# Optimization experiments

Measured on AMD Instinct MI355X. Metric: run time of the kernel, lower is better.

Reference implementation:

```python
import jax, jax.numpy as jnp
import numpy as np
import math

K = 4          # wavelet polynomial order
C = 16         # channel multiplier
MODES = 64     # retained Fourier modes (alpha)
L_LEVEL = 0    # coarsest level
B_SZ, N_SZ = 32, 8192
CK = C * K


def _get_filter_legendre(k):
    """Pure-numpy port of get_filter(base='legendre', k): Alpert multiwavelet filters."""
    from numpy.polynomial import legendre as npleg
    Poly = np.polynomial.Polynomial
    phi_coeff = np.zeros((k, k))
    phi_2x_coeff = np.zeros((k, k))
    for ki in range(k):
        c = np.zeros(ki + 1); c[ki] = 1.0
        base = Poly(npleg.leg2poly(c))
        p1 = base(Poly([-1.0, 2.0])).coef
        p2 = base(Poly([-1.0, 4.0])).coef
        phi_coeff[ki, :len(p1)] = np.sqrt(2 * ki + 1) * p1
        phi_2x_coeff[ki, :len(p2)] = np.sqrt(2.0) * np.sqrt(2 * ki + 1) * p2

    def proj_half(a, b, upper):
        # integral of poly(a)*poly(b) over [0,0.5] (upper=False) or [0.5,1] (upper=True)
        prod = np.convolve(a, b)
        prod[np.abs(prod) < 1e-8] = 0.0
        n = np.arange(len(prod))
        w = ((1.0 - np.power(0.5, n + 1)) if upper else np.power(0.5, n + 1)) / (n + 1)
        return (prod * w).sum()

    psi1_coeff = np.zeros((k, k)); psi2_coeff = np.zeros((k, k))
    for ki in range(k):
        psi1_coeff[ki, :] = phi_2x_coeff[ki, :]
        for i in range(k):
            p = proj_half(phi_2x_coeff[ki, :ki + 1], phi_coeff[i, :i + 1], False)
            psi1_coeff[ki, :] -= p * phi_coeff[i, :]
            psi2_coeff[ki, :] -= p * phi_coeff[i, :]
        for j in range(ki):
            p = proj_half(phi_2x_coeff[ki, :ki + 1], psi1_coeff[j, :], False)
            psi1_coeff[ki, :] -= p * psi1_coeff[j, :]
            psi2_coeff[ki, :] -= p * psi2_coeff[j, :]
        norm1 = proj_half(psi1_coeff[ki, :], psi1_coeff[ki, :], False)
        norm2 = proj_half(psi2_coeff[ki, :], psi2_coeff[ki, :], True)
        nrm = np.sqrt(norm1 + norm2)
        psi1_coeff[ki, :] /= nrm; psi2_coeff[ki, :] /= nrm
        psi1_coeff[np.abs(psi1_coeff) < 1e-8] = 0.0
        psi2_coeff[np.abs(psi2_coeff) < 1e-8] = 0.0

    t, w = npleg.leggauss(k)
    x_m = (t + 1.0) / 2.0; wm = w / 2.0     # Gauss-Legendre on [0,1]
    pv = np.polynomial.polynomial.polyval
    phi = lambda i, x: pv(x, phi_coeff[i])
    def psi(i, x):
        m = (x <= 0.5).astype(np.float64)
        return pv(x, psi1_coeff[i]) * m + pv(x, psi2_coeff[i]) * (1 - m)
    H0 = np.zeros((k, k)); H1 = np.zeros((k, k)); G0 = np.zeros((k, k)); G1 = np.zeros((k, k))
    s2 = np.sqrt(2.0)
    for ki in range(k):
        for kpi in range(k):
            H0[ki, kpi] = (wm * phi(ki, x_m / 2) * phi(kpi, x_m)).sum() / s2
            G0[ki, kpi] = (wm * psi(ki, x_m / 2) * phi(kpi, x_m)).sum() / s2
            H1[ki, kpi] = (wm * phi(ki, (x_m + 1) / 2) * phi(kpi, x_m)).sum() / s2
            G1[ki, kpi] = (wm * psi(ki, (x_m + 1) / 2) * phi(kpi, x_m)).sum() / s2
    for M in (H0, H1, G0, G1):
        M[np.abs(M) < 1e-8] = 0.0
    return H0, H1, G0, G1


_H0, _H1, _G0, _G1 = _get_filter_legendre(K)
# PHI0 = PHI1 = I for legendre, so H0r = H0 etc.
EC_S = jnp.asarray(np.concatenate((_H0.T, _H1.T), axis=0), dtype=jnp.float32)  # [2k,k]
EC_D = jnp.asarray(np.concatenate((_G0.T, _G1.T), axis=0), dtype=jnp.float32)
RC_E = jnp.asarray(np.concatenate((_H0, _G0), axis=0), dtype=jnp.float32)
RC_O = jnp.asarray(np.concatenate((_H1, _G1), axis=0), dtype=jnp.float32)


def _skft(x, w_re, w_im):
    """sparseKernelFT1d: FFT, truncated per-mode complex matmul, inverse FFT."""
    B, N, c, k = x.shape
    w = w_re + 1j * w_im                                   # [ck, ck, modes]
    xf = jnp.fft.rfft(x.reshape(B, N, c * k), axis=1)       # [B, N//2+1, ck]
    l = min(w.shape[-1], N // 2 + 1)
    out = jnp.einsum('bxi,iox->bxo', xf[:, :l, :], w[:, :, :l])
    out_full = jnp.zeros((B, N // 2 + 1, c * k), dtype=out.dtype).at[:, :l, :].set(out)
    y = jnp.fft.irfft(out_full, n=N, axis=1)
    return y.reshape(B, N, c, k)


def _mwt_cz1d(x, wA_re, wA_im, wB_re, wB_im, wC_re, wC_im, t0_w, t0_b):
    B, N, c, k = x.shape
    ns = int(math.floor(math.log2(N)))
    Ud, Us = [], []
    for _ in range(ns - L_LEVEL):
        # wavelet_transform
        xa = jnp.concatenate([x[:, ::2], x[:, 1::2]], axis=-1)   # [B, N/2, c, 2k]
        d = xa @ EC_D
        x = xa @ EC_S
        Ud.append(_skft(d, wA_re, wA_im) + _skft(x, wB_re, wB_im))
        Us.append(_skft(d, wC_re, wC_im))
    x = x @ t0_w.T + t0_b                                        # T0 linear on last dim k
    for i in range(ns - 1 - L_LEVEL, -1, -1):
        x = x + Us[i]
        x = jnp.concatenate([x, Ud[i]], axis=-1)                 # [B, M, c, 2k]
        x_e = x @ RC_E
        x_o = x @ RC_O
        M = x_e.shape[1]
        # interleave even/odd along the length axis
        x = jnp.stack([x_e, x_o], axis=2).reshape(B, 2 * M, c, k)
    return x


def setup_inputs() -> dict:
    key = jax.random.key(0)
    ks = jax.random.split(key, 8)
    scale = 1.0 / (CK * CK)
    return {
        'x': jax.random.normal(ks[0], (B_SZ, N_SZ, C, K), dtype=jnp.float32),
        'wA_re': scale * jax.random.uniform(ks[1], (CK, CK, MODES), dtype=jnp.float32),
        'wA_im': scale * jax.random.uniform(ks[2], (CK, CK, MODES), dtype=jnp.float32),
        'wB_re': scale * jax.random.uniform(ks[3], (CK, CK, MODES), dtype=jnp.float32),
        'wB_im': scale * jax.random.uniform(ks[4], (CK, CK, MODES), dtype=jnp.float32),
        'wC_re': scale * jax.random.uniform(ks[5], (CK, CK, MODES), dtype=jnp.float32),
        'wC_im': scale * jax.random.uniform(ks[6], (CK, CK, MODES), dtype=jnp.float32),
        't0_w': jax.random.normal(ks[7], (K, K), dtype=jnp.float32) / np.sqrt(K).astype(np.float32),
        't0_b': jnp.zeros((K,), dtype=jnp.float32),
    }


def reference(x, wA_re, wA_im, wB_re, wB_im, wC_re, wC_im, t0_w, t0_b):
    return _mwt_cz1d(x, wA_re, wA_im, wB_re, wB_im, wC_re, wC_im, t0_w, t0_b)
```

## Files before the change

kernel.cpp:

```cpp
#include <hip/hip_runtime.h>
#include <cmath>
#include <cstdint>


typedef __attribute__((ext_vector_type(8))) short bf16x8;
typedef __attribute__((ext_vector_type(4))) float f32x4;

struct Mat84 { float v[8][4]; };
struct Ptrs6 { const float* src[6]; uint16_t* dst[6]; };
struct TwLvls {
  int blkOff[14]; int Nl[13]; int l[13];
  unsigned long long fOff[13]; unsigned long long iOff[13];
};
struct FwdLvls {
  int blkOff[14]; int K[13]; int Kchunk[13];
  unsigned long long fOff[13]; unsigned long long bOff[13]; unsigned long long dOff[13];
};
struct MidLvls {
  int blkOff[14]; int l[13]; int nz[13];
  unsigned long long dOff[13]; unsigned long long sOff[13];
};
struct InvLvls {
  int blkOff[14]; int Nl[13]; int K2l[13];
  unsigned long long iOff[13]; unsigned long long sOff[13]; unsigned long long uOff[13];
};
struct DeepD { unsigned long long dsbOff[13]; };
struct DeepR { unsigned long long uOff[13]; };

__device__ __host__ inline uint16_t f2bf(float f) {
  union { float f; uint32_t u; } cv; cv.f = f;
  uint32_t u = cv.u;
  return (uint16_t)((u + 0x7fffu + ((u >> 16) & 1u)) >> 16);
}
__device__ inline float bf2f(uint16_t h) { return __uint_as_float((uint32_t)h << 16); }
__device__ inline uint32_t pack2(float a, float b) {
  return (uint32_t)f2bf(a) | ((uint32_t)f2bf(b) << 16);
}
__device__ inline bf16x8 negbf(bf16x8 x) {
  bf16x8 r;
#pragma unroll
  for (int j = 0; j < 8; j++) r[j] = (short)(x[j] ^ (short)0x8000);
  return r;
}
__device__ inline void gld_lds16(const uint16_t* g, uint16_t* l) {
  __builtin_amdgcn_global_load_lds(
      (const __attribute__((address_space(1))) void*)g,
      (__attribute__((address_space(3))) void*)l, 16, 0, 0);
}

static double proj_half_h(const double* a, const double* b, bool upper) {
  double prod[7] = {0, 0, 0, 0, 0, 0, 0};
  for (int i = 0; i < 4; i++)
    for (int j = 0; j < 4; j++)
      prod[i + j] += a[i] * b[j];
  for (int n = 0; n < 7; n++)
    if (fabs(prod[n]) < 1e-8) prod[n] = 0.0;
  double s = 0.0;
  for (int n = 0; n < 7; n++) {
    double w = upper ? (1.0 - pow(0.5, n + 1)) / (n + 1) : pow(0.5, n + 1) / (n + 1);
    s += prod[n] * w;
  }
  return s;
}
static double polyval4(const double* c, double x) {
  return c[0] + x * (c[1] + x * (c[2] + x * c[3]));
}

static void compute_filters(Mat84& ecs, Mat84& ecd, Mat84& rce, Mat84& rco) {
  const double leg[4][4] = {{1, 0, 0, 0}, {0, 1, 0, 0}, {-0.5, 0, 1.5, 0}, {0, -1.5, 0, 2.5}};
  double phi_c[4][4] = {}, phi2x_c[4][4] = {};
  const double s2 = sqrt(2.0);
  for (int ki = 0; ki < 4; ki++) {
    double a[4] = {0, 0, 0, 0};
    for (int j = 3; j >= 0; j--) {
      double na[4];
      for (int t = 0; t < 4; t++) { double v = -a[t]; if (t > 0) v += 2.0 * a[t - 1]; na[t] = v; }
      na[0] += leg[ki][j];
      for (int t = 0; t < 4; t++) a[t] = na[t];
    }
    for (int t = 0; t < 4; t++) phi_c[ki][t] = sqrt(2.0 * ki + 1.0) * a[t];
    double bb[4] = {0, 0, 0, 0};
    for (int j = 3; j >= 0; j--) {
      double nb[4];
      for (int t = 0; t < 4; t++) { double v = -bb[t]; if (t > 0) v += 4.0 * bb[t - 1]; nb[t] = v; }
      nb[0] += leg[ki][j];
      for (int t = 0; t < 4; t++) bb[t] = nb[t];
    }
    for (int t = 0; t < 4; t++) phi2x_c[ki][t] = s2 * sqrt(2.0 * ki + 1.0) * bb[t];
  }
  double psi1[4][4] = {}, psi2[4][4] = {};
  for (int ki = 0; ki < 4; ki++) {
    for (int t = 0; t < 4; t++) { psi1[ki][t] = phi2x_c[ki][t]; psi2[ki][t] = 0.0; }
    for (int i = 0; i < 4; i++) {
      double p = proj_half_h(phi2x_c[ki], phi_c[i], false);
      for (int t = 0; t < 4; t++) { psi1[ki][t] -= p * phi_c[i][t]; psi2[ki][t] -= p * phi_c[i][t]; }
    }
    for (int j = 0; j < ki; j++) {
      double p = proj_half_h(phi2x_c[ki], psi1[j], false);
      for (int t = 0; t < 4; t++) { psi1[ki][t] -= p * psi1[j][t]; psi2[ki][t] -= p * psi2[j][t]; }
    }
    double n1 = proj_half_h(psi1[ki], psi1[ki], false);
    double n2 = proj_half_h(psi2[ki], psi2[ki], true);
    double nr = sqrt(n1 + n2);
    for (int t = 0; t < 4; t++) { psi1[ki][t] /= nr; psi2[ki][t] /= nr; }
    for (int t = 0; t < 4; t++) {
      if (fabs(psi1[ki][t]) < 1e-8) psi1[ki][t] = 0.0;
      if (fabs(psi2[ki][t]) < 1e-8) psi2[ki][t] = 0.0;
    }
  }
  const double tq[4] = {-0.8611363115940526, -0.3399810435848563,
                        0.3399810435848563, 0.8611363115940526};
  const double wq[4] = {0.34785484513745385, 0.6521451548625461,
                        0.6521451548625461, 0.34785484513745385};
  double H0[4][4], H1[4][4], G0[4][4], G1[4][4];
  for (int ki = 0; ki < 4; ki++)
    for (int kp = 0; kp < 4; kp++) {
      double h0 = 0, h1 = 0, g0 = 0, g1 = 0;
      for (int m = 0; m < 4; m++) {
        double xm = (tq[m] + 1.0) * 0.5, wm = wq[m] * 0.5;
        double pk = polyval4(phi_c[kp], xm);
        h0 += wm * polyval4(phi_c[ki], xm * 0.5) * pk;
        h1 += wm * polyval4(phi_c[ki], (xm + 1.0) * 0.5) * pk;
        g0 += wm * polyval4(psi1[ki], xm * 0.5) * pk;
        g1 += wm * polyval4(psi2[ki], (xm + 1.0) * 0.5) * pk;
      }
      H0[ki][kp] = h0 / s2; H1[ki][kp] = h1 / s2; G0[ki][kp] = g0 / s2; G1[ki][kp] = g1 / s2;
    }
  for (int i = 0; i < 4; i++)
    for (int j = 0; j < 4; j++) {
      if (fabs(H0[i][j]) < 1e-8) H0[i][j] = 0.0;
      if (fabs(H1[i][j]) < 1e-8) H1[i][j] = 0.0;
      if (fabs(G0[i][j]) < 1e-8) G0[i][j] = 0.0;
      if (fabs(G1[i][j]) < 1e-8) G1[i][j] = 0.0;
    }
  for (int j = 0; j < 4; j++)
    for (int kk = 0; kk < 4; kk++) {
      ecs.v[j][kk]     = (float)H0[kk][j];
      ecs.v[j + 4][kk] = (float)H1[kk][j];
      ecd.v[j][kk]     = (float)G0[kk][j];
      ecd.v[j + 4][kk] = (float)G1[kk][j];
      rce.v[j][kk]     = (float)H0[j][kk];
      rce.v[j + 4][kk] = (float)G0[j][kk];
      rco.v[j][kk]     = (float)H1[j][kk];
      rco.v[j + 4][kk] = (float)G1[j][kk];
    }
}


__global__ void transpose_w(Ptrs6 p) {
  __shared__ float tile[64][65];
  int o = blockIdx.x, a = blockIdx.y;
  const float* w = p.src[a];
  uint16_t* wt = p.dst[a];
  int mm = threadIdx.x & 63, irow = threadIdx.x >> 6;
  for (int i = irow; i < 64; i += 4) tile[i][mm] = w[(((size_t)i * 64 + o) << 6) + mm];
  __syncthreads();
  int ii = threadIdx.x & 63, mrow = threadIdx.x >> 6;
  for (int mq = mrow; mq < 64; mq += 4)
    wt[(((size_t)mq * 64 + o) << 6) + ii] = f2bf(tile[ii][mq]);
}

__global__ void twiddle_all(uint16_t* __restrict__ FtwB, uint16_t* __restrict__ ItwB,
                            TwLvls tw) {
  int bx = blockIdx.x;
  int L = 0;
  while (L < 12 && bx >= tw.blkOff[L + 1]) L++;
  int Nl = tw.Nl[L], l = tw.l[L];
  int idx = (bx - tw.blkOff[L]) * 256 + threadIdx.x;
  if (idx >= 128 * Nl) return;
  uint16_t* Ftw = FtwB + tw.fOff[L];
  uint16_t* Itw = ItwB + tw.iOff[L];
  int n = idx % Nl, mm = idx / Nl;
  int m = (mm < l) ? mm : mm - l;
  int t = (m * n) & (Nl - 1);
  float ang = 6.2831853071795864769f * ((float)t / (float)Nl);
  float s, c;
  sincosf(ang, &s, &c);
  float fv = 0.f, iv = 0.f;
  float cm = (m == 0 || 2 * m == Nl) ? 1.0f : 2.0f;
  float sc = cm / (float)Nl;
  if (mm < l)          { fv = c;  iv = sc * c; }
  else if (mm < 2 * l) { fv = -s; iv = -sc * s; }
  Ftw[(size_t)mm * Nl + n] = f2bf(fv);
  Itw[(size_t)n * 128 + mm] = f2bf(iv);
}

__global__ __launch_bounds__(256) void decompose_kernel(
    const float* __restrict__ xin, float* __restrict__ s32,
    uint16_t* __restrict__ dsbfT, int Nl,
    Mat84 ecd, Mat84 ecs) {
  __shared__ uint32_t lds[128 * 34];
  int tid = threadIdx.x;
  int tile0 = blockIdx.x * 64;
  int b = blockIdx.y;
  int ci = tid & 15, nl = tid >> 4;
  float dall[4][4], sall[4][4];
#pragma unroll
  for (int jj = 0; jj < 4; jj++) {
    int n = tile0 + nl * 4 + jj;
    const float* r0 = xin + ((size_t)(b * 2 * Nl + 2 * n)) * 64 + ci * 4;
    float4 xe = *(const float4*)r0;
    float4 xo = *(const float4*)(r0 + 64);
    float xa[8] = {xe.x, xe.y, xe.z, xe.w, xo.x, xo.y, xo.z, xo.w};
    float d[4] = {0, 0, 0, 0}, s[4] = {0, 0, 0, 0};
#pragma unroll
    for (int j = 0; j < 8; j++) {
      float v = xa[j];
#pragma unroll
      for (int kk = 0; kk < 4; kk++) {
        d[kk] = fmaf(v, ecd.v[j][kk], d[kk]);
        s[kk] = fmaf(v, ecs.v[j][kk], s[kk]);
      }
    }
    *(float4*)&s32[((size_t)b * Nl + n) * 64 + ci * 4] = make_float4(s[0], s[1], s[2], s[3]);
#pragma unroll
    for (int kk = 0; kk < 4; kk++) { dall[jj][kk] = d[kk]; sall[jj][kk] = s[kk]; }
  }
#pragma unroll
  for (int kk = 0; kk < 4; kk++) {
    uint32_t d01 = pack2(dall[0][kk], dall[1][kk]);
    uint32_t d23 = pack2(dall[2][kk], dall[3][kk]);
    uint32_t s01 = pack2(sall[0][kk], sall[1][kk]);
    uint32_t s23 = pack2(sall[2][kk], sall[3][kk]);
    int cd = ci * 4 + kk;
    *(uint2*)&lds[cd * 34 + nl * 2] = make_uint2(d01, d23);
    *(uint2*)&lds[(64 + cd) * 34 + nl * 2] = make_uint2(s01, s23);
  }
  __syncthreads();
  uint32_t* outu = (uint32_t*)dsbfT;
  for (int e = tid; e < 128 * 32; e += 256) {
    int col = e >> 5, u = e & 31;
    uint32_t v = lds[col * 34 + u];
    outu[((((size_t)b * 128 + col) * Nl + tile0) >> 1) + u] = v;
  }
}

__global__ __launch_bounds__(256) void dec_deep(const float* __restrict__ sIn,
                                                uint16_t* __restrict__ DSbf,
                                                float* __restrict__ sFin,
                                                DeepD dd, Mat84 ecd, Mat84 ecs) {
  __shared__ float bufA[512 * 17];
  __shared__ float bufB[256 * 17];
  __shared__ uint16_t stg[32 * 256];
  int tid = threadIdx.x;
  int b = blockIdx.x >> 2, cc = blockIdx.x & 3;
  for (int e = tid; e < 512 * 4; e += 256) {
    int n = e >> 2, f4 = e & 3;
    float4 v = *(const float4*)&sIn[((size_t)b * 512 + n) * 64 + cc * 16 + f4 * 4];
    bufA[n * 17 + f4 * 4 + 0] = v.x;
    bufA[n * 17 + f4 * 4 + 1] = v.y;
    bufA[n * 17 + f4 * 4 + 2] = v.z;
    bufA[n * 17 + f4 * 4 + 3] = v.w;
  }
  __syncthreads();
  float* cur = bufA;
  float* nxt = bufB;
  int len = 512;
  for (int L = 4; L <= 12; L++) {
    int M = len >> 1;
    for (int e = tid; e < M * 4; e += 256) {
      int n = e >> 2, cl = e & 3;
      float xa[8];
#pragma unroll
      for (int j = 0; j < 4; j++) {
        xa[j]     = cur[(2 * n) * 17 + cl * 4 + j];
        xa[4 + j] = cur[(2 * n + 1) * 17 + cl * 4 + j];
      }
      float d[4] = {0, 0, 0, 0}, s[4] = {0, 0, 0, 0};
#pragma unroll
      for (int j = 0; j < 8; j++) {
        float v = xa[j];
#pragma unroll
        for (int kk = 0; kk < 4; kk++) {
          d[kk] = fmaf(v, ecd.v[j][kk], d[kk]);
          s[kk] = fmaf(v, ecs.v[j][kk], s[kk]);
        }
      }
#pragma unroll
      for (int kk = 0; kk < 4; kk++) {
        nxt[n * 17 + cl * 4 + kk] = s[kk];
        stg[(cl * 4 + kk) * 256 + n] = f2bf(d[kk]);
        stg[(16 + cl * 4 + kk) * 256 + n] = f2bf(s[kk]);
      }
    }
    __syncthreads();
    uint16_t* out = DSbf + dd.dsbOff[L];
    if (M >= 2) {
      int M2 = M >> 1;
      int lg = 31 - __builtin_clz(M2);
      uint32_t* outu = (uint32_t*)out;
      const uint32_t* stgu = (const uint32_t*)stg;
      for (int e = tid; e < 32 * M2; e += 256) {
        int r = e >> lg, u = e & (M2 - 1);
        int grow = (r < 16) ? (cc * 16 + r) : (64 + cc * 16 + (r - 16));
        outu[(((size_t)b * 128 + grow) * M >> 1) + u] = stgu[r * 128 + u];
      }
    } else {
      for (int e = tid; e < 32; e += 256) {
        int grow = (e < 16) ? (cc * 16 + e) : (64 + cc * 16 + (e - 16));
        out[(size_t)b * 128 + grow] = stg[e * 256];
      }
    }
    __syncthreads();
    float* t = cur; cur = nxt; nxt = t;
    len = M;
  }
  for (int e = tid; e < 16; e += 256) sFin[(size_t)b * 64 + cc * 16 + e] = cur[e];
}

__global__ __launch_bounds__(256) void fwd_all(const uint16_t* __restrict__ FtwB,
                                               const uint16_t* __restrict__ DSbfB,
                                               float* __restrict__ DfsB, FwdLvls fl) {
  __shared__ uint16_t As[2][4096];
  __shared__ uint16_t Bs[2][4096];
  int bx = blockIdx.x, L = 0;
  while (L < 12 && bx >= fl.blkOff[L + 1]) L++;
  int local = bx - fl.blkOff[L];
  int b = local & 31, z = local >> 5;
  int K = fl.K[L];
  int k0 = z * fl.Kchunk[L];
  int k1 = k0 + fl.Kchunk[L]; if (k1 > K) k1 = K;
  const uint16_t* A = FtwB + fl.fOff[L];
  const uint16_t* Bb = DSbfB + fl.bOff[L] + (size_t)b * 128 * K;
  int tid = threadIdx.x;
  int w = tid >> 6, lane = tid & 63;
  int wr = w >> 1, wc = w & 1;
  int lr = lane & 15, q = lane >> 4;
  f32x4 acc[4][4];
#pragma unroll
  for (int i = 0; i < 4; i++)
#pragma unroll
    for (int j = 0; j < 4; j++) acc[i][j] = (f32x4){0.f, 0.f, 0.f, 0.f};

  if (K >= 32) {
    int rsub = lane >> 2, g = lane & 3;
    int nsteps = (k1 - k0) >> 5;
    auto stage = [&](int buf, int kc) {
#pragma unroll
      for (int j = 0; j < 2; ++j) {
        int c = w * 2 + j;
        int row = c * 16 + rsub;
        gld_lds16(A + (size_t)row * K + kc + g * 8, &As[buf][c * 512]);
        gld_lds16(Bb + (size_t)row * K + kc + g * 8, &Bs[buf][c * 512]);
      }
    };
    stage(0, k0);
    __syncthreads();
    int cur = 0;
    for (int s = 0; s < nsteps; ++s) {
      if (s + 1 < nsteps) stage(cur ^ 1, k0 + ((s + 1) << 5));
      bf16x8 af[4], bfv[4];
#pragma unroll
      for (int t = 0; t < 4; t++) {
        af[t]  = *(const bf16x8*)&As[cur][(wr * 64 + t * 16 + lr) * 32 + q * 8];
        bfv[t] = *(const bf16x8*)&Bs[cur][(wc * 64 + t * 16 + lr) * 32 + q * 8];
      }
#pragma unroll
      for (int mt = 0; mt < 4; mt++)
#pragma unroll
        for (int nt = 0; nt < 4; nt++)
          acc[mt][nt] = __builtin_amdgcn_mfma_f32_16x16x32_bf16(af[mt], bfv[nt], acc[mt][nt], 0, 0, 0);
      __syncthreads();
      cur ^= 1;
    }
  } else {
    for (int s = tid; s < 512; s += 256) {
      int row = s >> 2, k8 = (s & 3) * 8;
      uint16_t ta[8], tb[8];
#pragma unroll
      for (int j = 0; j < 8; j++) {
        ta[j] = (k8 + j < k1) ? A[(size_t)row * K + k8 + j] : (uint16_t)0;
        tb[j] = (k8 + j < k1) ? Bb[(size_t)row * K + k8 + j] : (uint16_t)0;
      }
      *(uint4*)&As[0][row * 32 + k8] = *(const uint4*)ta;
      *(uint4*)&Bs[0][row * 32 + k8] = *(const uint4*)tb;
    }
    __syncthreads();
    bf16x8 af[4], bfv[4];
#pragma unroll
    for (int t = 0; t < 4; t++) {
      af[t]  = *(const bf16x8*)&As[0][(wr * 64 + t * 16 + lr) * 32 + q * 8];
      bfv[t] = *(const bf16x8*)&Bs[0][(wc * 64 + t * 16 + lr) * 32 + q * 8];
    }
#pragma unroll
    for (int mt = 0; mt < 4; mt++)
#pragma unroll
      for (int nt = 0; nt < 4; nt++)
        acc[mt][nt] = __builtin_amdgcn_mfma_f32_16x16x32_bf16(af[mt], bfv[nt], acc[mt][nt], 0, 0, 0);
  }

  float* Cb = DfsB + fl.dOff[L] + ((size_t)z * 32 + b) * 16384;
#pragma unroll
  for (int mt = 0; mt < 4; mt++) {
    int row0 = wr * 64 + mt * 16 + q * 4;
#pragma unroll
    for (int nt = 0; nt < 4; nt++) {
      int col = wc * 64 + nt * 16 + lr;
#pragma unroll
      for (int r = 0; r < 4; r++)
        Cb[(size_t)(row0 + r) * 128 + col] = acc[mt][nt][r];
    }
  }
}

__global__ __launch_bounds__(256) void middle_all(
    const float* __restrict__ DfsB,
    const uint16_t* __restrict__ wAr, const uint16_t* __restrict__ wAi,
    const uint16_t* __restrict__ wBr, const uint16_t* __restrict__ wBi,
    const uint16_t* __restrict__ wCr, const uint16_t* __restrict__ wCi,
    uint16_t* __restrict__ SpecTB, MidLvls ml) {
  __shared__ uint16_t Bs[6 * 64 * 64];
  __shared__ uint16_t As[8 * 32 * 64];
  int bx = blockIdx.x, L = 0;
  while (L < 12 && bx >= ml.blkOff[L + 1]) L++;
  int m = bx - ml.blkOff[L];
  int l = ml.l[L], nz = ml.nz[L];
  const float* Dfs = DfsB + ml.dOff[L];
  uint16_t* SpecT = SpecTB + ml.sOff[L];
  int tid = threadIdx.x;

#pragma unroll
  for (int a = 0; a < 6; a++) {
    const uint16_t* wpa = (a == 0) ? wAr : (a == 1) ? wAi : (a == 2) ? wBr
                        : (a == 3) ? wBi : (a == 4) ? wCr : wCi;
#pragma unroll
    for (int t0 = 0; t0 < 512; t0 += 256) {
      int t = t0 + tid;
      int o = t >> 3, g = t & 7;
      uint4 v = *(const uint4*)&wpa[(((size_t)m * 64 + o) << 6) + (g << 3)];
      *(uint4*)((char*)Bs + a * 8192 + o * 128 + (((g ^ (o & 7)) << 4))) = v;
    }
  }
  for (int e = tid; e < 2048; e += 256) {
    int c4 = (e & 31) * 4, r = (e >> 5) & 1, bb = e >> 6;
    size_t row = r ? (size_t)(l + m) : (size_t)m;
    float4 s = make_float4(0.f, 0.f, 0.f, 0.f);
    for (int z = 0; z < nz; z++) {
      float4 v = *(const float4*)&Dfs[((((size_t)z * 32 + bb) * 128 + row) << 7) + c4];
      s.x += v.x; s.y += v.y; s.z += v.z; s.w += v.w;
    }
    int vec = r + ((c4 >= 64) ? 2 : 0);
    int i0 = c4 & 63;
    float f[4] = {s.x, s.y, s.z, s.w};
    uint16_t hi[4], lo[4];
#pragma unroll
    for (int j = 0; j < 4; j++) {
      hi[j] = f2bf(f[j]);
      lo[j] = f2bf(f[j] - bf2f(hi[j]));
    }
    int g = i0 >> 3, w8 = (i0 & 7) * 2;
    char* ph = (char*)As + ((vec * 2 + 0) * 32 + bb) * 128 + ((g ^ (bb & 7)) << 4) + w8;
    char* pl = (char*)As + ((vec * 2 + 1) * 32 + bb) * 128 + ((g ^ (bb & 7)) << 4) + w8;
    *(uint2*)ph = make_uint2((uint32_t)hi[0] | ((uint32_t)hi[1] << 16),
                             (uint32_t)hi[2] | ((uint32_t)hi[3] << 16));
    *(uint2*)pl = make_uint2((uint32_t)lo[0] | ((uint32_t)lo[1] << 16),
                             (uint32_t)lo[2] | ((uint32_t)lo[3] << 16));
  }
  __syncthreads();

  int w = tid >> 6, lane = tid & 63;
  int lr = lane & 15, q = lane >> 4;
  f32x4 acc[2][4];
#pragma unroll
  for (int i = 0; i < 2; i++)
#pragma unroll
    for (int j = 0; j < 4; j++) acc[i][j] = (f32x4){0.f, 0.f, 0.f, 0.f};

  auto combo = [&](int v, int a, int ng) {
    bf16x8 bf[4][2];
#pragma unroll
    for (int nt = 0; nt < 4; nt++) {
      int o = nt * 16 + lr;
#pragma unroll
      for (int ks = 0; ks < 2; ks++) {
        int g = ks * 4 + q;
        bf[nt][ks] = *(const bf16x8*)((const char*)Bs + a * 8192 + o * 128 +
                                      ((g ^ (o & 7)) << 4));
      }
    }
#pragma unroll
    for (int p = 0; p < 2; p++) {
#pragma unroll
      for (int mt = 0; mt < 2; mt++) {
        int bb = mt * 16 + lr;
        const char* ab = (const char*)As + ((v * 2 + p) * 32 + bb) * 128;
        bf16x8 a0 = *(const bf16x8*)(ab + (((0 + q) ^ (bb & 7)) << 4));
        bf16x8 a1 = *(const bf16x8*)(ab + (((4 + q) ^ (bb & 7)) << 4));
        if (ng) { a0 = negbf(a0); a1 = negbf(a1); }
#pragma unroll
        for (int nt = 0; nt < 4; nt++) {
          acc[mt][nt] = __builtin_amdgcn_mfma_f32_16x16x32_bf16(a0, bf[nt][0], acc[mt][nt], 0, 0, 0);
          acc[mt][nt] = __builtin_amdgcn_mfma_f32_16x16x32_bf16(a1, bf[nt][1], acc[mt][nt], 0, 0, 0);
        }
      }
    }
  };
  if (w == 0) {
    combo(0, 0, 0); combo(1, 1, 1); combo(2, 2, 0); combo(3, 3, 1);
  } else if (w == 1) {
    combo(1, 0, 0); combo(0, 1, 0); combo(3, 2, 0); combo(2, 3, 0);
  } else if (w == 2) {
    combo(0, 4, 0); combo(1, 5, 1);
  } else {
    combo(1, 4, 0); combo(0, 5, 0);
  }

  int krow = (w & 1) ? (l + m) : m;
  int colbase = (w >= 2) ? 64 : 0;
#pragma unroll
  for (int mt = 0; mt < 2; mt++) {
#pragma unroll
    for (int nt = 0; nt < 4; nt++) {
#pragma unroll
      for (int r = 0; r < 4; r++) {
        int bb = mt * 16 + q * 4 + r;
        int oo = nt * 16 + lr;
        SpecT[((size_t)bb * 128 + colbase + oo) * 128 + krow] = f2bf(acc[mt][nt][r]);
      }
    }
  }
}

__global__ __launch_bounds__(256) void inv_all(const uint16_t* __restrict__ ItwB,
                                               const uint16_t* __restrict__ SpecTB,
                                               uint16_t* __restrict__ UdB,
                                               uint16_t* __restrict__ UsB, InvLvls il) {
  __shared__ uint16_t As[2][4096];
  __shared__ uint16_t Bs[2][4096];
  int bx = blockIdx.x, L = 0;
  while (L < 12 && bx >= il.blkOff[L + 1]) L++;
  int local = bx - il.blkOff[L];
  int b = local & 31, n0 = (local >> 5) * 128;
  int Nl = il.Nl[L], K2l = il.K2l[L];
  const uint16_t* A = ItwB + il.iOff[L];
  const uint16_t* Bb = SpecTB + il.sOff[L] + (size_t)b * 128 * 128;
  uint16_t* Ud = UdB + il.uOff[L];
  uint16_t* Us = UsB + il.uOff[L];
  int tid = threadIdx.x;
  int w = tid >> 6, lane = tid & 63;
  int wr = w >> 1, wc = w & 1;
  int lr = lane & 15, q = lane >> 4;
  f32x4 acc[4][4];
#pragma unroll
  for (int i = 0; i < 4; i++)
#pragma unroll
    for (int j = 0; j < 4; j++) acc[i][j] = (f32x4){0.f, 0.f, 0.f, 0.f};

  if (K2l == 128) {
    int rsub = lane >> 2, g = lane & 3;
    auto stage = [&](int buf, int kc) {
#pragma unroll
      for (int j = 0; j < 2; ++j) {
        int c = w * 2 + j;
        int row = c * 16 + rsub;
        gld_lds16(A + (size_t)(n0 + row) * 128 + kc + g * 8, &As[buf][c * 512]);
        gld_lds16(Bb + (size_t)row * 128 + kc + g * 8, &Bs[buf][c * 512]);
      }
    };
    stage(0, 0);
    __syncthreads();
    int cur = 0;
    for (int s = 0; s < 4; ++s) {
      if (s < 3) stage(cur ^ 1, (s + 1) << 5);
      bf16x8 af[4], bfv[4];
#pragma unroll
      for (int t = 0; t < 4; t++) {
        af[t]  = *(const bf16x8*)&As[cur][(wr * 64 + t * 16 + lr) * 32 + q * 8];
        bfv[t] = *(const bf16x8*)&Bs[cur][(wc * 64 + t * 16 + lr) * 32 + q * 8];
      }
#pragma unroll
      for (int mt = 0; mt < 4; mt++)
#pragma unroll
        for (int nt = 0; nt < 4; nt++)
          acc[mt][nt] = __builtin_amdgcn_mfma_f32_16x16x32_bf16(af[mt], bfv[nt], acc[mt][nt], 0, 0, 0);
      __syncthreads();
      cur ^= 1;
    }
  } else {
    for (int kc = 0; kc < 128; kc += 32) {
      for (int s = tid; s < 512; s += 256) {
        int row = s >> 2, k8 = (s & 3) * 8;
        int kg = kc + k8;
        *(uint4*)&As[0][row * 32 + k8] = *(const uint4*)&A[((size_t)(n0 + row)) * 128 + kg];
        uint16_t tb[8];
        if (kg + 8 <= K2l) {
          *(uint4*)tb = *(const uint4*)&Bb[(size_t)row * 128 + kg];
        } else {
#pragma unroll
          for (int j = 0; j < 8; j++)
            tb[j] = (kg + j < K2l) ? Bb[(size_t)row * 128 + kg + j] : (uint16_t)0;
        }
        *(uint4*)&Bs[0][row * 32 + k8] = *(const uint4*)tb;
      }
      __syncthreads();
      bf16x8 af[4], bfv[4];
#pragma unroll
      for (int t = 0; t < 4; t++) {
        af[t]  = *(const bf16x8*)&As[0][(wr * 64 + t * 16 + lr) * 32 + q * 8];
        bfv[t] = *(const bf16x8*)&Bs[0][(wc * 64 + t * 16 + lr) * 32 + q * 8];
      }
#pragma unroll
      for (int mt = 0; mt < 4; mt++)
#pragma unroll
        for (int nt = 0; nt < 4; nt++)
          acc[mt][nt] = __builtin_amdgcn_mfma_f32_16x16x32_bf16(af[mt], bfv[nt], acc[mt][nt], 0, 0, 0);
      __syncthreads();
    }
  }

#pragma unroll
  for (int mt = 0; mt < 4; mt++) {
    int row0 = wr * 64 + mt * 16 + q * 4;
#pragma unroll
    for (int nt = 0; nt < 4; nt++) {
      int col = wc * 64 + nt * 16 + lr;
#pragma unroll
      for (int r = 0; r < 4; r++) {
        int n = n0 + row0 + r;
        if (n < Nl) {
          uint16_t v = f2bf(acc[mt][nt][r]);
          if (col < 64) Ud[((size_t)b * Nl + n) * 64 + col] = v;
          else          Us[((size_t)b * Nl + n) * 64 + (col - 64)] = v;
        }
      }
    }
  }
}

__global__ __launch_bounds__(256) void recon_deep(const float* __restrict__ sFin,
                                                  const float* __restrict__ t0w,
                                                  const float* __restrict__ t0b,
                                                  const uint16_t* __restrict__ UdB,
                                                  const uint16_t* __restrict__ UsB,
                                                  float* __restrict__ xOut,
                                                  DeepR rl, Mat84 rce, Mat84 rco) {
  __shared__ float bufA[512 * 17];
  __shared__ float bufB[256 * 17];
  int tid = threadIdx.x;
  int b = blockIdx.x >> 2, cc = blockIdx.x & 3;
  if (tid < 16) {
    int cl = tid >> 2, kk = tid & 3;
    const float* sp = sFin + (size_t)b * 64 + cc * 16 + cl * 4;
    float v = t0b[kk];
#pragma unroll
    for (int k2 = 0; k2 < 4; k2++) v += t0w[kk * 4 + k2] * sp[k2];
    bufB[cl * 4 + kk] = v;
  }
  __syncthreads();
  float* cur = bufB;
  float* nxt = bufA;
  int M = 1;
  for (int i = 12; i >= 4; i--) {
    const uint16_t* Ud = UdB + rl.uOff[i];
    const uint16_t* Us = UsB + rl.uOff[i];
    for (int e = tid; e < M * 4; e += 256) {
      int n = e >> 2, cl = e & 3;
      size_t ua = ((size_t)b * M + n) * 64 + cc * 16 + cl * 4;
      ushort4 uu = *(const ushort4*)&Us[ua];
      ushort4 dd = *(const ushort4*)&Ud[ua];
      float t[8];
      t[0] = cur[n * 17 + cl * 4 + 0] + bf2f(uu.x);
      t[1] = cur[n * 17 + cl * 4 + 1] + bf2f(uu.y);
      t[2] = cur[n * 17 + cl * 4 + 2] + bf2f(uu.z);
      t[3] = cur[n * 17 + cl * 4 + 3] + bf2f(uu.w);
      t[4] = bf2f(dd.x); t[5] = bf2f(dd.y); t[6] = bf2f(dd.z); t[7] = bf2f(dd.w);
      float ev[4] = {0, 0, 0, 0}, ov[4] = {0, 0, 0, 0};
#pragma unroll
      for (int j = 0; j < 8; j++) {
        float v = t[j];
#pragma unroll
        for (int kk = 0; kk < 4; kk++) {
          ev[kk] = fmaf(v, rce.v[j][kk], ev[kk]);
          ov[kk] = fmaf(v, rco.v[j][kk], ov[kk]);
        }
      }
#pragma unroll
      for (int kk = 0; kk < 4; kk++) {
        nxt[(2 * n) * 17 + cl * 4 + kk] = ev[kk];
        nxt[(2 * n + 1) * 17 + cl * 4 + kk] = ov[kk];
      }
    }
    __syncthreads();
    float* t = cur; cur = nxt; nxt = t;
    M <<= 1;
  }
  for (int e = tid; e < 512 * 4; e += 256) {
    int n = e >> 2, f4 = e & 3;
    float4 v = make_float4(cur[n * 17 + f4 * 4 + 0], cur[n * 17 + f4 * 4 + 1],
                           cur[n * 17 + f4 * 4 + 2], cur[n * 17 + f4 * 4 + 3]);
    *(float4*)&xOut[((size_t)b * 512 + n) * 64 + cc * 16 + f4 * 4] = v;
  }
}

__global__ void recon_kernel(const float* __restrict__ x, const uint16_t* __restrict__ Ud,
                             const uint16_t* __restrict__ Us, float* __restrict__ out,
                             int M, int lgM, Mat84 rce, Mat84 rco) {
  int idx = blockIdx.x * 256 + threadIdx.x;
  int ci = idx & 15;
  int nb = idx >> 4;
  int m = nb & (M - 1);
  int b = nb >> lgM;
  if (b >= 32) return;
  size_t basei = ((size_t)b * M + m) * 64 + ci * 4;
  float4 xv = *(const float4*)&x[basei];
  ushort4 uu = *(const ushort4*)&Us[basei];
  ushort4 dd = *(const ushort4*)&Ud[basei];
  float t[8] = {xv.x + bf2f(uu.x), xv.y + bf2f(uu.y), xv.z + bf2f(uu.z), xv.w + bf2f(uu.w),
                bf2f(dd.x), bf2f(dd.y), bf2f(dd.z), bf2f(dd.w)};
  float e[4] = {0, 0, 0, 0}, o[4] = {0, 0, 0, 0};
#pragma unroll
  for (int j = 0; j < 8; j++) {
    float v = t[j];
#pragma unroll
    for (int kk = 0; kk < 4; kk++) {
      e[kk] = fmaf(v, rce.v[j][kk], e[kk]);
      o[kk] = fmaf(v, rco.v[j][kk], o[kk]);
    }
  }
  size_t ob = ((size_t)b * 2 * M + 2 * m) * 64 + ci * 4;
  *(float4*)&out[ob] = make_float4(e[0], e[1], e[2], e[3]);
  *(float4*)&out[ob + 64] = make_float4(o[0], o[1], o[2], o[3]);
}

extern "C" void kernel_launch(void* const* d_in, const int* in_sizes, int n_in,
                              void* d_out, int out_size, void* d_ws, size_t ws_size,
                              hipStream_t stream) {
  const float* x_in = (const float*)d_in[0];
  const float* t0w = (const float*)d_in[7];
  const float* t0b = (const float*)d_in[8];

  Mat84 ECS, ECD, RCE, RCO;
  compute_filters(ECS, ECD, RCE, RCO);

  int NlA[13], lA[13], nzA[13], KchA[13];
  size_t fOff[13], iOff[13], uOffA[13], dsbOff[13], dOff[13], sOff[13];
  size_t fo = 0, io = 0, uo = 0, db = 0, df = 0;
  for (int L = 0; L < 13; L++) {
    int Nl = 8192 >> (L + 1);
    int l = Nl / 2 + 1; if (l > 64) l = 64;
    NlA[L] = Nl; lA[L] = l;
    nzA[L] = (L == 0) ? 4 : (L == 1) ? 2 : 1;
    KchA[L] = Nl / nzA[L];
    fOff[L] = fo; fo += (size_t)128 * Nl;
    iOff[L] = io; io += (size_t)Nl * 128;
    uOffA[L] = uo; uo += (size_t)32 * 64 * Nl;
    dsbOff[L] = db; db += (size_t)32 * 128 * Nl;
    dOff[L] = df; df += (size_t)nzA[L] * 32 * 128 * 128;
    sOff[L] = (size_t)L * 32 * 128 * 128;
  }
  io += 128 * 128;

  char* base = (char*)d_ws;
  size_t off = 0;
  auto alloc = [&](size_t bytes) -> char* {
    char* p = base + off;
    off += (bytes + 255) & ~(size_t)255;
    return p;
  };
  float*    SA    = (float*)alloc((size_t)32 * 4096 * 64 * 4);
  float*    SB    = (float*)alloc((size_t)32 * 2048 * 64 * 4);
  float*    SC    = (float*)alloc((size_t)32 * 1024 * 64 * 4);
  float*    SD    = (float*)alloc((size_t)32 * 512 * 64 * 4);
  float*    SFin  = (float*)alloc((size_t)32 * 64 * 4);
  uint16_t* Ud    = (uint16_t*)alloc(uo * 2);
  uint16_t* Us    = (uint16_t*)alloc(uo * 2);
  float*    Dfs   = (float*)alloc(df * 4);
  uint16_t* SpecT = (uint16_t*)alloc((size_t)13 * 32 * 128 * 128 * 2);
  uint16_t* DSbf  = (uint16_t*)alloc(db * 2);
  uint16_t* Ftw   = (uint16_t*)alloc(fo * 2);
  uint16_t* Itw   = (uint16_t*)alloc(io * 2);
  uint16_t* wT[6];
  for (int a = 0; a < 6; a++) wT[a] = (uint16_t*)alloc((size_t)64 * 64 * 64 * 2);

  Ptrs6 p6;
  for (int a = 0; a < 6; a++) { p6.src[a] = (const float*)d_in[1 + a]; p6.dst[a] = wT[a]; }
  transpose_w<<<dim3(64, 6), 256, 0, stream>>>(p6);

  TwLvls tw;
  int bo = 0;
  for (int L = 0; L < 13; L++) {
    tw.blkOff[L] = bo;
    bo += (128 * NlA[L] + 255) / 256;
    tw.Nl[L] = NlA[L]; tw.l[L] = lA[L];
    tw.fOff[L] = fOff[L]; tw.iOff[L] = iOff[L];
  }
  tw.blkOff[13] = bo;
  twiddle_all<<<bo, 256, 0, stream>>>(Ftw, Itw, tw);

  {
    const float* srcs[4] = {x_in, SA, SB, SC};
    float* dsts[4] = {SA, SB, SC, SD};
    for (int L = 0; L < 4; L++) {
      int Nl = NlA[L];
      decompose_kernel<<<dim3(Nl / 64, 32), 256, 0, stream>>>(srcs[L], dsts[L],
                                                              DSbf + dsbOff[L], Nl, ECD, ECS);
    }
  }

  DeepD dd;
  for (int L = 0; L < 13; L++) dd.dsbOff[L] = dsbOff[L];
  dec_deep<<<128, 256, 0, stream>>>(SD, DSbf, SFin, dd, ECD, ECS);

  FwdLvls fl;
  bo = 0;
  for (int L = 0; L < 13; L++) {
    fl.blkOff[L] = bo; bo += 32 * nzA[L];
    fl.K[L] = NlA[L]; fl.Kchunk[L] = KchA[L];
    fl.fOff[L] = fOff[L]; fl.bOff[L] = dsbOff[L]; fl.dOff[L] = dOff[L];
  }
  fl.blkOff[13] = bo;
  fwd_all<<<bo, 256, 0, stream>>>(Ftw, DSbf, Dfs, fl);

  MidLvls ml;
  bo = 0;
  for (int L = 0; L < 13; L++) {
    ml.blkOff[L] = bo; bo += lA[L];
    ml.l[L] = lA[L]; ml.nz[L] = nzA[L];
    ml.dOff[L] = dOff[L]; ml.sOff[L] = sOff[L];
  }
  ml.blkOff[13] = bo;
  middle_all<<<bo, 256, 0, stream>>>(Dfs, wT[0], wT[1], wT[2], wT[3], wT[4], wT[5], SpecT, ml);

  InvLvls il;
  bo = 0;
  for (int L = 0; L < 13; L++) {
    il.blkOff[L] = bo; bo += ((NlA[L] + 127) / 128) * 32;
    il.Nl[L] = NlA[L]; il.K2l[L] = 2 * lA[L];
    il.iOff[L] = iOff[L]; il.sOff[L] = sOff[L]; il.uOff[L] = uOffA[L];
  }
  il.blkOff[13] = bo;
  inv_all<<<bo, 256, 0, stream>>>(Itw, SpecT, Ud, Us, il);

  DeepR rl;
  for (int L = 0; L < 13; L++) rl.uOff[L] = uOffA[L];
  recon_deep<<<128, 256, 0, stream>>>(SFin, t0w, t0b, Ud, Us, SD, rl, RCE, RCO);

  {
    float* xs[4] = {SD, SC, SB, SA};
    float* outs[4] = {SC, SB, SA, (float*)d_out};
    for (int t = 0; t < 4; t++) {
      int i = 3 - t;
      int M = NlA[i];
      int lg = 31 - __builtin_clz(M);
      recon_kernel<<<M * 2, 256, 0, stream>>>(xs[t], Ud + uOffA[i], Us + uOffA[i], outs[t],
                                              M, lg, RCE, RCO);
    }
  }
}
```

Before: 333.2 us.

## Swizzle LDS tiles and stage full K in inv_all with coalesced stores

Applies an XOR swizzle to LDS staging and fragment reads in the forward GEMM kernel so that row-strided reads stop conflicting on LDS banks. In inv_all's K=128 path, all of K is loaded into a 64KB swizzled LDS buffer in one shot, replacing the four-step double-buffered loop and removing the per-step barriers. The accumulators are then staged through padded LDS so the Ud/Us outputs can be written with 16-byte coalesced stores instead of scattered 2-byte stores. The larger LDS footprint may lower occupancy, and the new store path drops the n<Nl bounds check.

```diff
diff --git a/kernel.cpp b/kernel.cpp
--- a/kernel.cpp
+++ b/kernel.cpp
@@ -340,20 +340,22 @@
       for (int j = 0; j < 2; ++j) {
         int c = w * 2 + j;
         int row = c * 16 + rsub;
-        gld_lds16(A + (size_t)row * K + kc + g * 8, &As[buf][c * 512]);
-        gld_lds16(Bb + (size_t)row * K + kc + g * 8, &Bs[buf][c * 512]);
+        int gs = (g ^ ((row >> 1) & 3)) << 3;
+        gld_lds16(A + (size_t)row * K + kc + gs, &As[buf][c * 512]);
+        gld_lds16(Bb + (size_t)row * K + kc + gs, &Bs[buf][c * 512]);
       }
     };
     stage(0, k0);
     __syncthreads();
     int cur = 0;
+    int sw = (lr >> 1) & 3;
     for (int s = 0; s < nsteps; ++s) {
       if (s + 1 < nsteps) stage(cur ^ 1, k0 + ((s + 1) << 5));
       bf16x8 af[4], bfv[4];
 #pragma unroll
       for (int t = 0; t < 4; t++) {
-        af[t]  = *(const bf16x8*)&As[cur][(wr * 64 + t * 16 + lr) * 32 + q * 8];
-        bfv[t] = *(const bf16x8*)&Bs[cur][(wc * 64 + t * 16 + lr) * 32 + q * 8];
+        af[t]  = *(const bf16x8*)&As[cur][(wr * 64 + t * 16 + lr) * 32 + ((q ^ sw) << 3)];
+        bfv[t] = *(const bf16x8*)&Bs[cur][(wc * 64 + t * 16 + lr) * 32 + ((q ^ sw) << 3)];
       }
 #pragma unroll
       for (int mt = 0; mt < 4; mt++)
@@ -525,8 +527,7 @@
                                                const uint16_t* __restrict__ SpecTB,
                                                uint16_t* __restrict__ UdB,
                                                uint16_t* __restrict__ UsB, InvLvls il) {
-  __shared__ uint16_t As[2][4096];
-  __shared__ uint16_t Bs[2][4096];
+  __shared__ uint16_t lds[32768];
   int bx = blockIdx.x, L = 0;
   while (L < 12 && bx >= il.blkOff[L + 1]) L++;
   int local = bx - il.blkOff[L];
@@ -547,67 +548,87 @@
     for (int j = 0; j < 4; j++) acc[i][j] = (f32x4){0.f, 0.f, 0.f, 0.f};
 
   if (K2l == 128) {
-    int rsub = lane >> 2, g = lane & 3;
-    auto stage = [&](int buf, int kc) {
-#pragma unroll
-      for (int j = 0; j < 2; ++j) {
-        int c = w * 2 + j;
-        int row = c * 16 + rsub;
-        gld_lds16(A + (size_t)(n0 + row) * 128 + kc + g * 8, &As[buf][c * 512]);
-        gld_lds16(Bb + (size_t)row * 128 + kc + g * 8, &Bs[buf][c * 512]);
-      }
-    };
-    stage(0, 0);
-    __syncthreads();
-    int cur = 0;
-    for (int s = 0; s < 4; ++s) {
-      if (s < 3) stage(cur ^ 1, (s + 1) << 5);
+    uint16_t* As0 = lds;
+    uint16_t* Bs0 = lds + 16384;
+    int rsub = lane >> 4, p = lane & 15;
+#pragma unroll
+    for (int i = 0; i < 8; i++) {
+      int rowb = w * 32 + i * 4;
+      int row = rowb + rsub;
+      int gs = (p ^ (row & 7)) << 3;
+      gld_lds16(A + (size_t)(n0 + row) * 128 + gs, As0 + rowb * 128);
+      gld_lds16(Bb + (size_t)row * 128 + gs, Bs0 + rowb * 128);
+    }
+    __syncthreads();
+    int sw = lr & 7;
+#pragma unroll
+    for (int kc = 0; kc < 4; kc++) {
       bf16x8 af[4], bfv[4];
 #pragma unroll
       for (int t = 0; t < 4; t++) {
-        af[t]  = *(const bf16x8*)&As[cur][(wr * 64 + t * 16 + lr) * 32 + q * 8];
-        bfv[t] = *(const bf16x8*)&Bs[cur][(wc * 64 + t * 16 + lr) * 32 + q * 8];
+        int g = kc * 4 + q;
+        af[t]  = *(const bf16x8*)&As0[(wr * 64 + t * 16 + lr) * 128 + ((g ^ sw) << 3)];
+        bfv[t] = *(const bf16x8*)&Bs0[(wc * 64 + t * 16 + lr) * 128 + ((g ^ sw) << 3)];
       }
 #pragma unroll
       for (int mt = 0; mt < 4; mt++)
 #pragma unroll
         for (int nt = 0; nt < 4; nt++)
           acc[mt][nt] = __builtin_amdgcn_mfma_f32_16x16x32_bf16(af[mt], bfv[nt], acc[mt][nt], 0, 0, 0);
-      __syncthreads();
-      cur ^= 1;
-    }
-  } else {
-    for (int kc = 0; kc < 128; kc += 32) {
-      for (int s = tid; s < 512; s += 256) {
-        int row = s >> 2, k8 = (s & 3) * 8;
-        int kg = kc + k8;
-        *(uint4*)&As[0][row * 32 + k8] = *(const uint4*)&A[((size_t)(n0 + row)) * 128 + kg];
-        uint16_t tb[8];
-        if (kg + 8 <= K2l) {
-          *(uint4*)tb = *(const uint4*)&Bb[(size_t)row * 128 + kg];
-        } else {
-#pragma unroll
-          for (int j = 0; j < 8; j++)
-            tb[j] = (kg + j < K2l) ? Bb[(size_t)row * 128 + kg + j] : (uint16_t)0;
-        }
-        *(uint4*)&Bs[0][row * 32 + k8] = *(const uint4*)tb;
-      }
-      __syncthreads();
-      bf16x8 af[4], bfv[4];
-#pragma unroll
-      for (int t = 0; t < 4; t++) {
-        af[t]  = *(const bf16x8*)&As[0][(wr * 64 + t * 16 + lr) * 32 + q * 8];
-        bfv[t] = *(const bf16x8*)&Bs[0][(wc * 64 + t * 16 + lr) * 32 + q * 8];
-      }
-#pragma unroll
-      for (int mt = 0; mt < 4; mt++)
-#pragma unroll
-        for (int nt = 0; nt < 4; nt++)
-          acc[mt][nt] = __builtin_amdgcn_mfma_f32_16x16x32_bf16(af[mt], bfv[nt], acc[mt][nt], 0, 0, 0);
-      __syncthreads();
-    }
-  }
-
+    }
+    __syncthreads();
+#pragma unroll
+    for (int mt = 0; mt < 4; mt++)
+#pragma unroll
+      for (int nt = 0; nt < 4; nt++)
+#pragma unroll
+        for (int r = 0; r < 4; r++)
+          lds[(wr * 64 + mt * 16 + q * 4 + r) * 132 + wc * 64 + nt * 16 + lr] =
+              f2bf(acc[mt][nt][r]);
+    __syncthreads();
+    uint16_t* Udb = Ud + ((size_t)b * Nl + n0) * 64;
+    uint16_t* Usb = Us + ((size_t)b * Nl + n0) * 64;
+#pragma unroll
+    for (int i = 0; i < 4; i++) {
+      int f = i * 256 + tid;
+      int row = f >> 3, c8 = (f & 7) * 8;
+      *(uint4*)(Udb + (size_t)f * 8) = *(const uint4*)&lds[row * 132 + c8];
+      *(uint4*)(Usb + (size_t)f * 8) = *(const uint4*)&lds[row * 132 + 64 + c8];
+    }
+    return;
+  }
+
+  uint16_t* As0 = lds;
+  uint16_t* Bs0 = lds + 4096;
+  for (int kc = 0; kc < 128; kc += 32) {
+    for (int s = tid; s < 512; s += 256) {
+      int row = s >> 2, k8 = (s & 3) * 8;
+      int kg = kc + k8;
+      *(uint4*)&As0[row * 32 + k8] = *(const uint4*)&A[((size_t)(n0 + row)) * 128 + kg];
+      uint16_t tb[8];
+      if (kg + 8 <= K2l) {
+        *(uint4*)tb = *(const uint4*)&Bb[(size_t)row * 128 + kg];
+      } else {
+#pragma unroll
+        for (int j = 0; j < 8; j++)
+          tb[j] = (kg + j < K2l) ? Bb[(size_t)row * 128 + kg + j] : (uint16_t)0;
+      }
+      *(uint4*)&Bs0[row * 32 + k8] = *(const uint4*)tb;
+    }
+    __syncthreads();
+    bf16x8 af[4], bfv[4];
+#pragma unroll
+    for (int t = 0; t < 4; t++) {
+      af[t]  = *(const bf16x8*)&As0[(wr * 64 + t * 16 + lr) * 32 + q * 8];
+      bfv[t] = *(const bf16x8*)&Bs0[(wc * 64 + t * 16 + lr) * 32 + q * 8];
+    }
+#pragma unroll
+    for (int mt = 0; mt < 4; mt++)
+#pragma unroll
+      for (int nt = 0; nt < 4; nt++)
+        acc[mt][nt] = __builtin_amdgcn_mfma_f32_16x16x32_bf16(af[mt], bfv[nt], acc[mt][nt], 0, 0, 0);
+    __syncthreads();
+  }
 #pragma unroll
   for (int mt = 0; mt < 4; mt++) {
     int row0 = wr * 64 + mt * 16 + q * 4;
```

New measurement: 331.4 us. No clear change (-0.6%).
